# Kernel tuning notes

Measured on AMD Instinct MI355X. Metric: run time of the kernel, lower is better.

The kernel has to match this reference:

```python
import jax, jax.numpy as jnp
import numpy as np


def setup_inputs() -> dict:
    key = jax.random.key(0)
    k1, k2, k3, k4, k5 = jax.random.split(key, 5)
    E, D, G = 2_000_000, 64, 8192
    return {
        "h_edges": jax.random.normal(k1, (E, D), dtype=jnp.float32),
        "h_metadata": jax.random.normal(k2, (G, 128), dtype=jnp.float32),
        "h_attended": jax.random.normal(k3, (G, 128), dtype=jnp.float32),
        "h_current_node": jax.random.normal(k4, (G, 128), dtype=jnp.float32),
        "edge_batch": jnp.sort(jax.random.randint(k5, (E,), 0, G, dtype=jnp.int32)),
        "num_graphs": G,
    }


def reference(h_edges, h_metadata, h_attended, h_current_node, edge_batch, num_graphs):
    G = num_graphs
    # per-segment counts (scatter 'mean' divides by count, empty segments -> 0)
    counts = jax.ops.segment_sum(jnp.ones_like(edge_batch, dtype=h_edges.dtype),
                                 edge_batch, num_segments=G)  # [G]
    safe_counts = jnp.maximum(counts, 1.0)[:, None]  # avoid div-by-zero

    seg_sum = jax.ops.segment_sum(h_edges, edge_batch, num_segments=G)  # [G, D]
    h_mean = seg_sum / safe_counts

    nonempty = (counts > 0)[:, None]
    h_max = jnp.where(nonempty, jax.ops.segment_max(h_edges, edge_batch, num_segments=G), 0.0)
    h_min = jnp.where(nonempty, jax.ops.segment_min(h_edges, edge_batch, num_segments=G), 0.0)

    # variance: mean of squared deviation from the per-segment mean
    dev2 = (h_edges - h_mean[edge_batch]) ** 2  # [E, D]
    h_var = jax.ops.segment_sum(dev2, edge_batch, num_segments=G) / safe_counts

    return jnp.concatenate(
        [h_metadata, h_mean, h_var, h_max, h_min, h_attended, h_current_node], axis=1)
```

## Files before the change

### kernel.cpp

```cpp
#include <hip/hip_runtime.h>
#include <cfloat>

__global__ __launch_bounds__(256) void seg_bounds_kernel(
    const int* __restrict__ eb, int E, int G, int* __restrict__ seg)
{
    int g = blockIdx.x * blockDim.x + threadIdx.x;
    if (g > G) return;
    int lo = 0, hi = E;
    while (lo < hi) {
        int mid = (lo + hi) >> 1;
        if (eb[mid] < g) lo = mid + 1; else hi = mid;
    }
    seg[g] = lo;
}

#define ACC(v)                                                            \
    do {                                                                  \
        sum.x += (v).x; sum.y += (v).y; sum.z += (v).z; sum.w += (v).w;   \
        sq.x += (v).x * (v).x; sq.y += (v).y * (v).y;                     \
        sq.z += (v).z * (v).z; sq.w += (v).w * (v).w;                     \
        mx.x = fmaxf(mx.x, (v).x); mx.y = fmaxf(mx.y, (v).y);             \
        mx.z = fmaxf(mx.z, (v).z); mx.w = fmaxf(mx.w, (v).w);             \
        mn.x = fminf(mn.x, (v).x); mn.y = fminf(mn.y, (v).y);             \
        mn.z = fminf(mn.z, (v).z); mn.w = fminf(mn.w, (v).w);             \
    } while (0)

__global__ __launch_bounds__(256) void graph_embed_kernel(
    const float4* __restrict__ edges,
    const float4* __restrict__ meta,
    const float4* __restrict__ att,
    const float4* __restrict__ cur,
    const int*    __restrict__ seg,
    float4*       __restrict__ out)
{
    const int g   = blockIdx.x;
    const int tid = threadIdx.x;
    const int f   = tid & 15;
    const int r   = tid >> 4;

    {
        const size_t ob = (size_t)g * 160;
        const size_t ib = (size_t)g * 32;
        if (tid < 32)      out[ob +        tid      ] = meta[ib + tid];
        else if (tid < 64) out[ob +  96 + (tid - 32)] = att [ib + (tid - 32)];
        else if (tid < 96) out[ob + 128 + (tid - 64)] = cur [ib + (tid - 64)];
    }

    const int start = seg[g];
    const int end   = seg[g + 1];
    const int count = end - start;

    float4 sum = make_float4(0.f, 0.f, 0.f, 0.f);
    float4 sq  = make_float4(0.f, 0.f, 0.f, 0.f);
    float4 mx  = make_float4(-FLT_MAX, -FLT_MAX, -FLT_MAX, -FLT_MAX);
    float4 mn  = make_float4( FLT_MAX,  FLT_MAX,  FLT_MAX,  FLT_MAX);

    int row = start + r;
    for (; row + 48 < end; row += 64) {
        float4 v0 = edges[(size_t)(row     ) * 16 + f];
        float4 v1 = edges[(size_t)(row + 16) * 16 + f];
        float4 v2 = edges[(size_t)(row + 32) * 16 + f];
        float4 v3 = edges[(size_t)(row + 48) * 16 + f];
        ACC(v0); ACC(v1); ACC(v2); ACC(v3);
    }
    for (; row < end; row += 16) {
        float4 v = edges[(size_t)row * 16 + f];
        ACC(v);
    }

    __shared__ float4 s_sum[16][16];
    __shared__ float4 s_sq [16][16];
    __shared__ float4 s_mx [16][16];
    __shared__ float4 s_mn [16][16];
    s_sum[r][f] = sum; s_sq[r][f] = sq; s_mx[r][f] = mx; s_mn[r][f] = mn;
    __syncthreads();

    #pragma unroll
    for (int step = 8; step >= 1; step >>= 1) {
        if (r < step) {
            float4 a = s_sum[r][f], b = s_sum[r + step][f];
            a.x += b.x; a.y += b.y; a.z += b.z; a.w += b.w;
            s_sum[r][f] = a;
            float4 c = s_sq[r][f], d = s_sq[r + step][f];
            c.x += d.x; c.y += d.y; c.z += d.z; c.w += d.w;
            s_sq[r][f] = c;
            float4 e = s_mx[r][f], h = s_mx[r + step][f];
            e.x = fmaxf(e.x, h.x); e.y = fmaxf(e.y, h.y);
            e.z = fmaxf(e.z, h.z); e.w = fmaxf(e.w, h.w);
            s_mx[r][f] = e;
            float4 p = s_mn[r][f], q = s_mn[r + step][f];
            p.x = fminf(p.x, q.x); p.y = fminf(p.y, q.y);
            p.z = fminf(p.z, q.z); p.w = fminf(p.w, q.w);
            s_mn[r][f] = p;
        }
        __syncthreads();
    }

    if (tid < 16) {
        float4 S = s_sum[0][tid], Q = s_sq[0][tid];
        float4 X = s_mx[0][tid],  N = s_mn[0][tid];
        float4 mean, var;
        if (count > 0) {
            const float inv = 1.0f / (float)count;
            mean.x = S.x * inv; mean.y = S.y * inv;
            mean.z = S.z * inv; mean.w = S.w * inv;
            var.x = fmaxf(Q.x * inv - mean.x * mean.x, 0.f);
            var.y = fmaxf(Q.y * inv - mean.y * mean.y, 0.f);
            var.z = fmaxf(Q.z * inv - mean.z * mean.z, 0.f);
            var.w = fmaxf(Q.w * inv - mean.w * mean.w, 0.f);
        } else {
            mean = make_float4(0.f, 0.f, 0.f, 0.f);
            var = mean; X = mean; N = mean;
        }
        float4* orow = out + (size_t)g * 160;
        orow[32 + tid] = mean;
        orow[48 + tid] = var;
        orow[64 + tid] = X;
        orow[80 + tid] = N;
    }
}

extern "C" void kernel_launch(void* const* d_in, const int* in_sizes, int n_in,
                              void* d_out, int out_size, void* d_ws, size_t ws_size,
                              hipStream_t stream)
{
    const float* h_edges = (const float*)d_in[0];
    const float* h_meta  = (const float*)d_in[1];
    const float* h_att   = (const float*)d_in[2];
    const float* h_cur   = (const float*)d_in[3];
    const int*   e_batch = (const int*)d_in[4];

    const int E = in_sizes[4];
    const int G = in_sizes[1] / 128;

    int* seg = (int*)d_ws;

    seg_bounds_kernel<<<(G + 1 + 255) / 256, 256, 0, stream>>>(e_batch, E, G, seg);

    graph_embed_kernel<<<G, 256, 0, stream>>>(
        (const float4*)h_edges, (const float4*)h_meta, (const float4*)h_att,
        (const float4*)h_cur, seg, (float4*)d_out);
}
```

Before: 119.4 us.

## Process four graphs per block with wave-shuffle reduction and streaming segment bounds

Replaces the per-graph binary search with a streaming pass over edge_batch that writes segment boundaries at transitions. Each block now handles four graphs, reducing the partial statistics with cross-lane shuffles, then a small double-buffered shared-memory stage with one barrier per graph. The final statistics are spread across 64 threads instead of 16. This cuts block count and shared-memory reduction barriers, but lowers parallelism to G/4 blocks and makes graphs within a block run serially.

```diff
diff --git a/kernel.cpp b/kernel.cpp
--- a/kernel.cpp
+++ b/kernel.cpp
@@ -1,17 +1,40 @@
 #include <hip/hip_runtime.h>
 #include <cfloat>
 
-__global__ __launch_bounds__(256) void seg_bounds_kernel(
+#define GPB 4
+
+__global__ __launch_bounds__(256) void seg_bounds_stream(
     const int* __restrict__ eb, int E, int G, int* __restrict__ seg)
 {
-    int g = blockIdx.x * blockDim.x + threadIdx.x;
-    if (g > G) return;
-    int lo = 0, hi = E;
-    while (lo < hi) {
-        int mid = (lo + hi) >> 1;
-        if (eb[mid] < g) lo = mid + 1; else hi = mid;
-    }
-    seg[g] = lo;
+    int i = blockIdx.x * blockDim.x + threadIdx.x;
+    if (i >= E) return;
+    int b0 = eb[i];
+    int b1 = (i + 1 < E) ? eb[i + 1] : G;
+    if (i == 0)
+        for (int g = 0; g <= b0; ++g) seg[g] = 0;
+    for (int g = b0; g < b1; ++g) seg[g + 1] = i + 1;
+}
+
+__device__ __forceinline__ float4 wred_add(float4 v) {
+    v.x += __shfl_xor(v.x, 16); v.y += __shfl_xor(v.y, 16);
+    v.z += __shfl_xor(v.z, 16); v.w += __shfl_xor(v.w, 16);
+    v.x += __shfl_xor(v.x, 32); v.y += __shfl_xor(v.y, 32);
+    v.z += __shfl_xor(v.z, 32); v.w += __shfl_xor(v.w, 32);
+    return v;
+}
+__device__ __forceinline__ float4 wred_max(float4 v) {
+    v.x = fmaxf(v.x, __shfl_xor(v.x, 16)); v.y = fmaxf(v.y, __shfl_xor(v.y, 16));
+    v.z = fmaxf(v.z, __shfl_xor(v.z, 16)); v.w = fmaxf(v.w, __shfl_xor(v.w, 16));
+    v.x = fmaxf(v.x, __shfl_xor(v.x, 32)); v.y = fmaxf(v.y, __shfl_xor(v.y, 32));
+    v.z = fmaxf(v.z, __shfl_xor(v.z, 32)); v.w = fmaxf(v.w, __shfl_xor(v.w, 32));
+    return v;
+}
+__device__ __forceinline__ float4 wred_min(float4 v) {
+    v.x = fminf(v.x, __shfl_xor(v.x, 16)); v.y = fminf(v.y, __shfl_xor(v.y, 16));
+    v.z = fminf(v.z, __shfl_xor(v.z, 16)); v.w = fminf(v.w, __shfl_xor(v.w, 16));
+    v.x = fminf(v.x, __shfl_xor(v.x, 32)); v.y = fminf(v.y, __shfl_xor(v.y, 32));
+    v.z = fminf(v.z, __shfl_xor(v.z, 32)); v.w = fminf(v.w, __shfl_xor(v.w, 32));
+    return v;
 }
 
 #define ACC(v)                                                            \
@@ -31,92 +54,114 @@
     const float4* __restrict__ att,
     const float4* __restrict__ cur,
     const int*    __restrict__ seg,
-    float4*       __restrict__ out)
+    float4*       __restrict__ out,
+    int G)
 {
-    const int g   = blockIdx.x;
-    const int tid = threadIdx.x;
-    const int f   = tid & 15;
-    const int r   = tid >> 4;
+    const int tid  = threadIdx.x;
+    const int g4   = blockIdx.x * GPB;
+    const int f    = tid & 15;
+    const int r    = tid >> 4;
+    const int lane = tid & 63;
+    const int w    = tid >> 6;
 
-    {
-        const size_t ob = (size_t)g * 160;
-        const size_t ib = (size_t)g * 32;
-        if (tid < 32)      out[ob +        tid      ] = meta[ib + tid];
-        else if (tid < 64) out[ob +  96 + (tid - 32)] = att [ib + (tid - 32)];
-        else if (tid < 96) out[ob + 128 + (tid - 64)] = cur [ib + (tid - 64)];
+    for (int t = tid; t < 96 * GPB; t += 256) {
+        const int j = t / 96, k = t % 96;
+        const size_t ob = (size_t)(g4 + j) * 160;
+        const size_t ib = (size_t)(g4 + j) * 32;
+        const int sel = k >> 5, kk = k & 31;
+        if (sel == 0)      out[ob +       kk] = meta[ib + kk];
+        else if (sel == 1) out[ob +  96 + kk] = att [ib + kk];
+        else               out[ob + 128 + kk] = cur [ib + kk];
     }
 
-    const int start = seg[g];
-    const int end   = seg[g + 1];
-    const int count = end - start;
+    int starts[GPB + 1];
+    #pragma unroll
+    for (int k = 0; k <= GPB; ++k)
+        starts[k] = seg[min(g4 + k, G)];
 
-    float4 sum = make_float4(0.f, 0.f, 0.f, 0.f);
-    float4 sq  = make_float4(0.f, 0.f, 0.f, 0.f);
-    float4 mx  = make_float4(-FLT_MAX, -FLT_MAX, -FLT_MAX, -FLT_MAX);
-    float4 mn  = make_float4( FLT_MAX,  FLT_MAX,  FLT_MAX,  FLT_MAX);
-
-    int row = start + r;
-    for (; row + 48 < end; row += 64) {
-        float4 v0 = edges[(size_t)(row     ) * 16 + f];
-        float4 v1 = edges[(size_t)(row + 16) * 16 + f];
-        float4 v2 = edges[(size_t)(row + 32) * 16 + f];
-        float4 v3 = edges[(size_t)(row + 48) * 16 + f];
-        ACC(v0); ACC(v1); ACC(v2); ACC(v3);
-    }
-    for (; row < end; row += 16) {
-        float4 v = edges[(size_t)row * 16 + f];
-        ACC(v);
-    }
-
-    __shared__ float4 s_sum[16][16];
-    __shared__ float4 s_sq [16][16];
-    __shared__ float4 s_mx [16][16];
-    __shared__ float4 s_mn [16][16];
-    s_sum[r][f] = sum; s_sq[r][f] = sq; s_mx[r][f] = mx; s_mn[r][f] = mn;
-    __syncthreads();
+    __shared__ float4 sred[2][4][4][16];
 
     #pragma unroll
-    for (int step = 8; step >= 1; step >>= 1) {
-        if (r < step) {
-            float4 a = s_sum[r][f], b = s_sum[r + step][f];
-            a.x += b.x; a.y += b.y; a.z += b.z; a.w += b.w;
-            s_sum[r][f] = a;
-            float4 c = s_sq[r][f], d = s_sq[r + step][f];
-            c.x += d.x; c.y += d.y; c.z += d.z; c.w += d.w;
-            s_sq[r][f] = c;
-            float4 e = s_mx[r][f], h = s_mx[r + step][f];
-            e.x = fmaxf(e.x, h.x); e.y = fmaxf(e.y, h.y);
-            e.z = fmaxf(e.z, h.z); e.w = fmaxf(e.w, h.w);
-            s_mx[r][f] = e;
-            float4 p = s_mn[r][f], q = s_mn[r + step][f];
-            p.x = fminf(p.x, q.x); p.y = fminf(p.y, q.y);
-            p.z = fminf(p.z, q.z); p.w = fminf(p.w, q.w);
-            s_mn[r][f] = p;
+    for (int j = 0; j < GPB; ++j) {
+        if (g4 + j >= G) break;
+        const int start = starts[j];
+        const int end   = starts[j + 1];
+        const int count = end - start;
+
+        float4 sum = make_float4(0.f, 0.f, 0.f, 0.f);
+        float4 sq  = make_float4(0.f, 0.f, 0.f, 0.f);
+        float4 mx  = make_float4(-FLT_MAX, -FLT_MAX, -FLT_MAX, -FLT_MAX);
+        float4 mn  = make_float4( FLT_MAX,  FLT_MAX,  FLT_MAX,  FLT_MAX);
+
+        int row = start + r;
+        for (; row + 48 < end; row += 64) {
+            float4 v0 = edges[(size_t)(row     ) * 16 + f];
+            float4 v1 = edges[(size_t)(row + 16) * 16 + f];
+            float4 v2 = edges[(size_t)(row + 32) * 16 + f];
+            float4 v3 = edges[(size_t)(row + 48) * 16 + f];
+            ACC(v0); ACC(v1); ACC(v2); ACC(v3);
+        }
+        for (; row < end; row += 16) {
+            float4 v = edges[(size_t)row * 16 + f];
+            ACC(v);
+        }
+
+        sum = wred_add(sum);
+        sq  = wred_add(sq);
+        mx  = wred_max(mx);
+        mn  = wred_min(mn);
+
+        const int buf = j & 1;
+        if (lane < 16) {
+            sred[buf][0][w][lane] = sum;
+            sred[buf][1][w][lane] = sq;
+            sred[buf][2][w][lane] = mx;
+            sred[buf][3][w][lane] = mn;
         }
         __syncthreads();
-    }
 
-    if (tid < 16) {
-        float4 S = s_sum[0][tid], Q = s_sq[0][tid];
-        float4 X = s_mx[0][tid],  N = s_mn[0][tid];
-        float4 mean, var;
-        if (count > 0) {
-            const float inv = 1.0f / (float)count;
-            mean.x = S.x * inv; mean.y = S.y * inv;
-            mean.z = S.z * inv; mean.w = S.w * inv;
-            var.x = fmaxf(Q.x * inv - mean.x * mean.x, 0.f);
-            var.y = fmaxf(Q.y * inv - mean.y * mean.y, 0.f);
-            var.z = fmaxf(Q.z * inv - mean.z * mean.z, 0.f);
-            var.w = fmaxf(Q.w * inv - mean.w * mean.w, 0.f);
-        } else {
-            mean = make_float4(0.f, 0.f, 0.f, 0.f);
-            var = mean; X = mean; N = mean;
+        if (tid < 64) {
+            float4 res;
+            if (count == 0) {
+                res = make_float4(0.f, 0.f, 0.f, 0.f);
+            } else if (r < 2) {
+                float4 S = sred[buf][0][0][f];
+                float4 b1 = sred[buf][0][1][f], b2 = sred[buf][0][2][f], b3 = sred[buf][0][3][f];
+                S.x += b1.x + b2.x + b3.x; S.y += b1.y + b2.y + b3.y;
+                S.z += b1.z + b2.z + b3.z; S.w += b1.w + b2.w + b3.w;
+                const float inv = 1.0f / (float)count;
+                float4 mean = make_float4(S.x * inv, S.y * inv, S.z * inv, S.w * inv);
+                if (r == 0) {
+                    res = mean;
+                } else {
+                    float4 Q = sred[buf][1][0][f];
+                    float4 c1 = sred[buf][1][1][f], c2 = sred[buf][1][2][f], c3 = sred[buf][1][3][f];
+                    Q.x += c1.x + c2.x + c3.x; Q.y += c1.y + c2.y + c3.y;
+                    Q.z += c1.z + c2.z + c3.z; Q.w += c1.w + c2.w + c3.w;
+                    res.x = fmaxf(Q.x * inv - mean.x * mean.x, 0.f);
+                    res.y = fmaxf(Q.y * inv - mean.y * mean.y, 0.f);
+                    res.z = fmaxf(Q.z * inv - mean.z * mean.z, 0.f);
+                    res.w = fmaxf(Q.w * inv - mean.w * mean.w, 0.f);
+                }
+            } else if (r == 2) {
+                float4 X = sred[buf][2][0][f];
+                float4 d1 = sred[buf][2][1][f], d2 = sred[buf][2][2][f], d3 = sred[buf][2][3][f];
+                X.x = fmaxf(fmaxf(X.x, d1.x), fmaxf(d2.x, d3.x));
+                X.y = fmaxf(fmaxf(X.y, d1.y), fmaxf(d2.y, d3.y));
+                X.z = fmaxf(fmaxf(X.z, d1.z), fmaxf(d2.z, d3.z));
+                X.w = fmaxf(fmaxf(X.w, d1.w), fmaxf(d2.w, d3.w));
+                res = X;
+            } else {
+                float4 N = sred[buf][3][0][f];
+                float4 e1 = sred[buf][3][1][f], e2 = sred[buf][3][2][f], e3 = sred[buf][3][3][f];
+                N.x = fminf(fminf(N.x, e1.x), fminf(e2.x, e3.x));
+                N.y = fminf(fminf(N.y, e1.y), fminf(e2.y, e3.y));
+                N.z = fminf(fminf(N.z, e1.z), fminf(e2.z, e3.z));
+                N.w = fminf(fminf(N.w, e1.w), fminf(e2.w, e3.w));
+                res = N;
+            }
+            out[(size_t)(g4 + j) * 160 + 32 + tid] = res;
         }
-        float4* orow = out + (size_t)g * 160;
-        orow[32 + tid] = mean;
-        orow[48 + tid] = var;
-        orow[64 + tid] = X;
-        orow[80 + tid] = N;
     }
 }
 
@@ -135,9 +180,10 @@
 
     int* seg = (int*)d_ws;
 
-    seg_bounds_kernel<<<(G + 1 + 255) / 256, 256, 0, stream>>>(e_batch, E, G, seg);
+    seg_bounds_stream<<<(E + 255) / 256, 256, 0, stream>>>(e_batch, E, G, seg);
 
-    graph_embed_kernel<<<G, 256, 0, stream>>>(
+    const int nblk = (G + GPB - 1) / GPB;
+    graph_embed_kernel<<<nblk, 256, 0, stream>>>(
         (const float4*)h_edges, (const float4*)h_meta, (const float4*)h_att,
-        (const float4*)h_cur, seg, (float4*)d_out);
+        (const float4*)h_cur, seg, (float4*)d_out, G);
 }
```

After: 120.2 us. No clear change (+0.7%).
